# Kernel tuning notes

Measured on AMD Instinct MI355X. Metric: run time of the kernel, lower is better.

## Reference

```python
import jax, jax.numpy as jnp
import numpy as np

T = 2048
D_MODEL = 4096
N_HEADS = 32
N_GROUPS = 8
HEAD_DIM = 128


def _rope_tables(tokens, head_dim, base=10000.0):
    inv_freq = 1.0 / (base ** (np.arange(0, head_dim, 2, dtype=np.float32) / head_dim))
    pos = np.arange(tokens, dtype=np.float32)
    freqs = np.einsum('t,d->td', pos, inv_freq)          # [T, D/2]
    emb = np.concatenate([freqs, freqs], axis=-1)         # [T, D]
    return jnp.asarray(np.cos(emb)), jnp.asarray(np.sin(emb))


def setup_inputs() -> dict:
    key = jax.random.key(0)
    k1, k2, k3 = jax.random.split(key, 3)
    x = jax.random.normal(k1, (T, D_MODEL), dtype=jnp.float32)
    w_qkv = jax.random.normal(k2, (D_MODEL, (N_HEADS + 2 * N_GROUPS) * HEAD_DIM), dtype=jnp.float32) * 0.02
    w_out = jax.random.normal(k3, (N_HEADS * HEAD_DIM, D_MODEL), dtype=jnp.float32) * 0.02
    cos, sin = _rope_tables(T, HEAD_DIM)
    mask = jnp.tril(jnp.ones((T, T), dtype=bool))  # causal: [suffix_tokens, total_tokens]
    return {"x": x, "w_qkv": w_qkv, "w_out": w_out, "cos": cos, "sin": sin, "mask": mask}


def _rotate_half(u):
    u1, u2 = jnp.split(u, 2, axis=-1)
    return jnp.concatenate([-u2, u1], axis=-1)


def _apply_rope(u, cos, sin):
    # u: [tokens, heads, head_dim]; cos/sin: [tokens, head_dim]
    c = cos[:, None, :]
    s = sin[:, None, :]
    return u * c + _rotate_half(u) * s


def reference(x, w_qkv, w_out, cos, sin, mask):
    group_dim = N_HEADS // N_GROUPS
    qkv = x @ w_qkv                                        # [T, (H+2G)*D]
    q, k, v = jnp.split(qkv, [N_HEADS * HEAD_DIM, (N_HEADS + N_GROUPS) * HEAD_DIM], axis=-1)
    q = q.reshape(T, N_HEADS, HEAD_DIM)
    k = k.reshape(T, N_GROUPS, HEAD_DIM)
    v = v.reshape(T, N_GROUPS, HEAD_DIM)
    q = _apply_rope(q, cos, sin)
    k = _apply_rope(k, cos, sin)
    # GQA: group queries -> [T, G, group_dim, D]
    qg = q.reshape(T, N_GROUPS, group_dim, HEAD_DIM)
    scale = 1.0 / jnp.sqrt(jnp.asarray(HEAD_DIM, dtype=q.dtype))
    scores = jnp.einsum('tghd,sgd->ghts', qg, k) * scale   # [G, gd, T, S]
    neg = jnp.asarray(jnp.finfo(scores.dtype).min, scores.dtype)
    scores = jnp.where(mask[None, None, :, :], scores, neg)
    probs = jax.nn.softmax(scores, axis=-1)
    out = jnp.einsum('ghts,sgd->tghd', probs, v)           # [T, G, gd, D]
    out = out.reshape(T, N_HEADS * HEAD_DIM)
    return out @ w_out                                     # [T, model_dim]
```

## Files before the change

kernel.cpp:

```cpp
#include <hip/hip_runtime.h>
#include <cstdint>
#include <cstddef>

#define TT   2048
#define DM   4096
#define NH   32
#define NG   8
#define HD   128
#define QKVN 6144
#define KOFF 4096
#define VOFF 5120

typedef __attribute__((ext_vector_type(8))) short bf16x8;
typedef __attribute__((ext_vector_type(4))) float f32x4;
typedef unsigned short u16;

__device__ __forceinline__ u16 f2b(float f) {
  unsigned u = __builtin_bit_cast(unsigned, f);
  u += 0x7fffu + ((u >> 16) & 1u);
  return (u16)(u >> 16);
}
__device__ __forceinline__ float b2f(u16 s) {
  unsigned u = ((unsigned)s) << 16;
  return __builtin_bit_cast(float, u);
}

__device__ __forceinline__ void gload_lds16(const void* g, void* l) {
  __builtin_amdgcn_global_load_lds(
      (const __attribute__((address_space(1))) unsigned int*)g,
      (__attribute__((address_space(3))) unsigned int*)l,
      16, 0, 0);
}

__global__ __launch_bounds__(256) void cvt_f32_bf16(
    const float* __restrict__ src, u16* __restrict__ dst, int n) {
  for (int i = (blockIdx.x * 256 + threadIdx.x) * 4; i < n; i += gridDim.x * 256 * 4) {
    float4 v = *(const float4*)(src + i);
    ushort4 o;
    o.x = f2b(v.x); o.y = f2b(v.y); o.z = f2b(v.z); o.w = f2b(v.w);
    *(ushort4*)(dst + i) = o;
  }
}

__global__ __launch_bounds__(256) void transpose_cvt(
    const float* __restrict__ src, u16* __restrict__ dst, int R, int C) {
  __shared__ __align__(16) u16 tile[64 * 68];
  const int rb = blockIdx.y * 64, cb = blockIdx.x * 64;
  const int tid = threadIdx.x;
#pragma unroll
  for (int it = 0; it < 4; ++it) {
    const int idx = it * 256 + tid;
    const int r = idx >> 4, c4 = (idx & 15) * 4;
    const float4 v = *(const float4*)(src + (size_t)(rb + r) * C + cb + c4);
    tile[(c4 + 0) * 68 + r] = f2b(v.x);
    tile[(c4 + 1) * 68 + r] = f2b(v.y);
    tile[(c4 + 2) * 68 + r] = f2b(v.z);
    tile[(c4 + 3) * 68 + r] = f2b(v.w);
  }
  __syncthreads();
#pragma unroll
  for (int it = 0; it < 4; ++it) {
    const int idx = it * 256 + tid;
    const int c = idx >> 4, r4 = (idx & 15) * 4;
    const ushort4 o = *(const ushort4*)&tile[c * 68 + r4];
    *(ushort4*)(dst + (size_t)(cb + c) * R + rb + r4) = o;
  }
}

template <int WN, bool OUT_BF16>
__global__ __launch_bounds__(512) void gemm8p(
    const u16* __restrict__ A, const u16* __restrict__ Bt, void* __restrict__ Cout,
    int M, int N, int K) {
  __shared__ __align__(16) u16 sA[2][128 * 64];
  __shared__ __align__(16) u16 sB[2][WN * 64 * 64];
  const int tid = threadIdx.x;
  const int wid = tid >> 6, lane = tid & 63;
  const int lane15 = lane & 15, laneh = lane >> 4;
  const int wm = wid >> 2, wn = wid & 3;
  const int bid = blockIdx.x;
  const int xcd = bid & 7, j = bid >> 3;
  const int m0 = ((xcd >> 1) * 4 + (j >> 3)) * 128;
  const int n0 = ((xcd & 1) * 8 + (j & 7)) * (WN * 64);
  const int xorL = (lane15 & 7) << 3;

  f32x4 acc[4][WN];
#pragma unroll
  for (int m = 0; m < 4; ++m)
#pragma unroll
    for (int n = 0; n < WN; ++n)
#pragma unroll
      for (int r = 0; r < 4; ++r) acc[m][n][r] = 0.f;

  auto stageA = [&](int buf, int t) {
    const int k0 = t << 6;
#pragma unroll
    for (int i = 0; i < 2; ++i) {
      const int ebase = (wid * 2 + i) * 512;
      const int e = ebase + lane * 8;
      const int row = e >> 6;
      const int col = (e & 63) ^ ((row & 7) << 3);
      gload_lds16(A + (size_t)(m0 + row) * K + k0 + col, &sA[buf][ebase]);
    }
  };
  auto stageB = [&](int buf, int t) {
    const int k0 = t << 6;
#pragma unroll
    for (int i = 0; i < WN; ++i) {
      const int ebase = (wid * WN + i) * 512;
      const int e = ebase + lane * 8;
      const int row = e >> 6;
      const int col = (e & 63) ^ ((row & 7) << 3);
      gload_lds16(Bt + (size_t)(n0 + row) * K + k0 + col, &sB[buf][ebase]);
    }
  };

  const int NT = K >> 6;
  stageA(0, 0);
  stageB(0, 0);
  stageA(1, 1);
  asm volatile("s_waitcnt vmcnt(2)");
  __builtin_amdgcn_s_barrier();

  for (int u = 0; u < NT; ++u) {
    const int cur = u & 1;
    bf16x8 af[4][2], bfr[WN][2];
#pragma unroll
    for (int m = 0; m < 4; ++m)
#pragma unroll
      for (int ks = 0; ks < 2; ++ks)
        af[m][ks] = *(const bf16x8*)&sA[cur][(wm * 64 + m * 16 + lane15) * 64 +
                                            ((ks * 32 + laneh * 8) ^ xorL)];
#pragma unroll
    for (int n = 0; n < WN / 2; ++n)
#pragma unroll
      for (int ks = 0; ks < 2; ++ks)
        bfr[n][ks] = *(const bf16x8*)&sB[cur][(wn * (WN * 16) + n * 16 + lane15) * 64 +
                                             ((ks * 32 + laneh * 8) ^ xorL)];
    if (u + 1 < NT) stageB(cur ^ 1, u + 1);
    __builtin_amdgcn_sched_barrier(0);
    __builtin_amdgcn_s_setprio(1);
#pragma unroll
    for (int ks = 0; ks < 2; ++ks)
#pragma unroll
      for (int m = 0; m < 4; ++m)
#pragma unroll
        for (int n = 0; n < WN / 2; ++n)
          acc[m][n] = __builtin_amdgcn_mfma_f32_16x16x32_bf16(af[m][ks], bfr[n][ks], acc[m][n], 0, 0, 0);
    __builtin_amdgcn_s_setprio(0);
    __builtin_amdgcn_s_barrier();
#pragma unroll
    for (int n = WN / 2; n < WN; ++n)
#pragma unroll
      for (int ks = 0; ks < 2; ++ks)
        bfr[n][ks] = *(const bf16x8*)&sB[cur][(wn * (WN * 16) + n * 16 + lane15) * 64 +
                                             ((ks * 32 + laneh * 8) ^ xorL)];
    if (u + 2 < NT) stageA(cur, u + 2);
    __builtin_amdgcn_sched_barrier(0);
    __builtin_amdgcn_s_setprio(1);
#pragma unroll
    for (int ks = 0; ks < 2; ++ks)
#pragma unroll
      for (int m = 0; m < 4; ++m)
#pragma unroll
        for (int n = WN / 2; n < WN; ++n)
          acc[m][n] = __builtin_amdgcn_mfma_f32_16x16x32_bf16(af[m][ks], bfr[n][ks], acc[m][n], 0, 0, 0);
    __builtin_amdgcn_s_setprio(0);
    if (u + 2 < NT) asm volatile("s_waitcnt vmcnt(2)");
    else            asm volatile("s_waitcnt vmcnt(0)");
    __builtin_amdgcn_s_barrier();
  }
#pragma unroll
  for (int m = 0; m < 4; ++m)
#pragma unroll
    for (int n = 0; n < WN; ++n)
#pragma unroll
      for (int r = 0; r < 4; ++r) {
        const int row = m0 + wm * 64 + m * 16 + laneh * 4 + r;
        const int col = n0 + wn * (WN * 16) + n * 16 + lane15;
        const float v = acc[m][n][r];
        if (OUT_BF16) ((u16*)Cout)[(size_t)row * N + col] = f2b(v);
        else          ((float*)Cout)[(size_t)row * N + col] = v;
      }
}

__global__ __launch_bounds__(256) void rope_rearrange(
    const u16* __restrict__ qkv, const float* __restrict__ cosT,
    const float* __restrict__ sinT, u16* __restrict__ Qr, u16* __restrict__ Kr) {
  const int u = blockIdx.x * 4 + (threadIdx.x >> 6);
  const int lane = threadIdx.x & 63;
  const int t = u & (TT - 1);
  const int e = u >> 11;
  const u16* in;
  u16* outp;
  if (e < NH) {
    in = qkv + (size_t)t * QKVN + e * HD;
    outp = Qr + ((size_t)e * TT + t) * HD;
  } else {
    const int g = e - NH;
    in = qkv + (size_t)t * QKVN + KOFF + g * HD;
    outp = Kr + ((size_t)g * TT + t) * HD;
  }
  const float u1 = b2f(in[lane]), u2 = b2f(in[lane + 64]);
  const float c1 = cosT[t * HD + lane], s1 = sinT[t * HD + lane];
  const float c2 = cosT[t * HD + lane + 64], s2 = sinT[t * HD + lane + 64];
  outp[lane]      = f2b(u1 * c1 - u2 * s1);
  outp[lane + 64] = f2b(u2 * c2 + u1 * s2);
}

__global__ __launch_bounds__(256) void vtrans(
    const u16* __restrict__ qkv, u16* __restrict__ VT) {
  __shared__ u16 tile[64][66];
  const int g = blockIdx.z;
  const int t0 = blockIdx.x * 64, d0 = blockIdx.y * 64;
  const int tid = threadIdx.x;
#pragma unroll
  for (int it = 0; it < 16; ++it) {
    int idx = it * 256 + tid;
    int i = idx >> 6, j = idx & 63;
    tile[i][j] = qkv[(size_t)(t0 + i) * QKVN + VOFF + g * HD + d0 + j];
  }
  __syncthreads();
#pragma unroll
  for (int it = 0; it < 16; ++it) {
    int idx = it * 256 + tid;
    int j = idx >> 6, i = idx & 63;
    VT[((size_t)g * HD + d0 + j) * TT + t0 + i] = tile[i][j];
  }
}

__global__ __launch_bounds__(512)
__attribute__((amdgpu_waves_per_eu(1, 2)))
void attn(
    const u16* __restrict__ Qr, const u16* __restrict__ Kr,
    const u16* __restrict__ VT, u16* __restrict__ AO) {
  __shared__ __align__(16) u16 sK[2][128 * 128];
  __shared__ __align__(16) u16 sV[2][128 * 128];
  __shared__ __align__(16) u16 sP[8][32 * 64];
  const int bid = blockIdx.x;
  const int swz = (bid & 7) * 32 + (bid >> 3);
  const int h = swz >> 3, p = swz & 7;
  const int g = h >> 2;
  const int tid = threadIdx.x, wid = tid >> 6, lane = tid & 63;
  const int lane15 = lane & 15, laneh = lane >> 4;
  const int qw = wid >> 1, sw = wid & 1;
  const int xorL = (lane15 & 7) << 3;
  const u16* Qh = Qr + (size_t)h * TT * HD;
  const u16* Kg = Kr + (size_t)g * TT * HD;
  const u16* Vg = VT + (size_t)g * HD * TT;
  const float scale = 0.08838834764831845f;
  float* mlbuf = (float*)&sP[0][0];
  float* obuf  = (float*)&sK[0][0];

  auto stageKV = [&](int buf, int kv) {
#pragma unroll
    for (int i = 0; i < 4; ++i) {
      const int ebase = (wid * 4 + i) * 512;
      const int e = ebase + lane * 8;
      const int row = e >> 7;
      const int col = (e & 127) ^ ((row & 7) << 3);
      gload_lds16(Kg + (size_t)(kv * 128 + row) * HD + col, &sK[buf][ebase]);
      gload_lds16(Vg + (size_t)row * TT + kv * 128 + col, &sV[buf][ebase]);
    }
  };

  for (int pass = 0; pass < 2; ++pass) {
    const int qt = pass ? (15 - p) : p;
    bf16x8 qf[2][4];
    const int qrow0 = qt * 128 + qw * 32;
#pragma unroll
    for (int m = 0; m < 2; ++m)
#pragma unroll
      for (int ks = 0; ks < 4; ++ks)
        qf[m][ks] = *(const bf16x8*)(Qh + (size_t)(qrow0 + m * 16 + lane15) * HD + ks * 32 + laneh * 8);

    f32x4 acc[2][8];
    float mrow[2][4], lrow[2][4];
#pragma unroll
    for (int m = 0; m < 2; ++m) {
#pragma unroll
      for (int n = 0; n < 8; ++n)
#pragma unroll
        for (int r = 0; r < 4; ++r) acc[m][n][r] = 0.f;
#pragma unroll
      for (int r = 0; r < 4; ++r) { mrow[m][r] = -1e30f; lrow[m][r] = 0.f; }
    }

    stageKV(0, 0);
    for (int kv = 0; kv <= qt; ++kv) {
      const int cur = kv & 1;
      if (kv < qt) stageKV(cur ^ 1, kv + 1);
      __builtin_amdgcn_sched_barrier(0);
      if (kv < qt) asm volatile("s_waitcnt vmcnt(8)");
      else         asm volatile("s_waitcnt vmcnt(0)");
      __builtin_amdgcn_s_barrier();

      f32x4 s[2][4];
#pragma unroll
      for (int m = 0; m < 2; ++m)
#pragma unroll
        for (int n = 0; n < 4; ++n)
#pragma unroll
          for (int r = 0; r < 4; ++r) s[m][n][r] = 0.f;
      __builtin_amdgcn_s_setprio(1);
#pragma unroll
      for (int ks = 0; ks < 4; ++ks) {
        bf16x8 kf[4];
#pragma unroll
        for (int n = 0; n < 4; ++n)
          kf[n] = *(const bf16x8*)&sK[cur][(sw * 64 + n * 16 + lane15) * 128 +
                                          ((ks * 32 + laneh * 8) ^ xorL)];
#pragma unroll
        for (int m = 0; m < 2; ++m)
#pragma unroll
          for (int n = 0; n < 4; ++n)
            s[m][n] = __builtin_amdgcn_mfma_f32_16x16x32_bf16(qf[m][ks], kf[n], s[m][n], 0, 0, 0);
      }
      __builtin_amdgcn_s_setprio(0);

      if (kv == qt) {
#pragma unroll
        for (int m = 0; m < 2; ++m)
#pragma unroll
          for (int n = 0; n < 4; ++n)
#pragma unroll
            for (int r = 0; r < 4; ++r) {
              const int ql = qw * 32 + m * 16 + laneh * 4 + r;
              const int sl = sw * 64 + n * 16 + lane15;
              s[m][n][r] = (sl > ql) ? -1e30f : s[m][n][r] * scale;
            }
      } else {
#pragma unroll
        for (int m = 0; m < 2; ++m)
#pragma unroll
          for (int n = 0; n < 4; ++n)
#pragma unroll
            for (int r = 0; r < 4; ++r) s[m][n][r] *= scale;
      }
#pragma unroll
      for (int m = 0; m < 2; ++m)
#pragma unroll
        for (int r = 0; r < 4; ++r) {
          float pm = s[m][0][r];
#pragma unroll
          for (int n = 1; n < 4; ++n) pm = fmaxf(pm, s[m][n][r]);
          pm = fmaxf(pm, __shfl_xor(pm, 1));
          pm = fmaxf(pm, __shfl_xor(pm, 2));
          pm = fmaxf(pm, __shfl_xor(pm, 4));
          pm = fmaxf(pm, __shfl_xor(pm, 8));
          const float mnew = fmaxf(mrow[m][r], pm);
          const float corr = __expf(mrow[m][r] - mnew);
          mrow[m][r] = mnew;
          float ps = 0.f;
#pragma unroll
          for (int n = 0; n < 4; ++n) {
            const float pr = __expf(s[m][n][r] - mnew);
            s[m][n][r] = pr;
            ps += pr;
          }
          ps += __shfl_xor(ps, 1); ps += __shfl_xor(ps, 2);
          ps += __shfl_xor(ps, 4); ps += __shfl_xor(ps, 8);
          lrow[m][r] = lrow[m][r] * corr + ps;
#pragma unroll
          for (int n = 0; n < 8; ++n) acc[m][n][r] *= corr;
        }
#pragma unroll
      for (int m = 0; m < 2; ++m)
#pragma unroll
        for (int n = 0; n < 4; ++n)
#pragma unroll
          for (int r = 0; r < 4; ++r) {
            const int prow = m * 16 + laneh * 4 + r;
            const int pcol = (n * 16 + lane15) ^ ((prow & 7) << 3);
            sP[wid][prow * 64 + pcol] = f2b(s[m][n][r]);
          }
      __builtin_amdgcn_s_setprio(1);
#pragma unroll
      for (int ks = 0; ks < 2; ++ks) {
        bf16x8 pf[2];
#pragma unroll
        for (int m = 0; m < 2; ++m)
          pf[m] = *(const bf16x8*)&sP[wid][(m * 16 + lane15) * 64 + ((ks * 32 + laneh * 8) ^ xorL)];
#pragma unroll
        for (int nh = 0; nh < 2; ++nh) {
          bf16x8 vf[4];
#pragma unroll
          for (int n = 0; n < 4; ++n)
            vf[n] = *(const bf16x8*)&sV[cur][((nh * 4 + n) * 16 + lane15) * 128 +
                                            ((sw * 64 + ks * 32 + laneh * 8) ^ xorL)];
#pragma unroll
          for (int m = 0; m < 2; ++m)
#pragma unroll
            for (int n = 0; n < 4; ++n)
              acc[m][nh * 4 + n] =
                  __builtin_amdgcn_mfma_f32_16x16x32_bf16(pf[m], vf[n], acc[m][nh * 4 + n], 0, 0, 0);
        }
      }
      __builtin_amdgcn_s_setprio(0);
      __builtin_amdgcn_s_barrier();
    }

    if (lane15 == 0) {
#pragma unroll
      for (int m = 0; m < 2; ++m)
#pragma unroll
        for (int r = 0; r < 4; ++r) {
          const int row = m * 16 + laneh * 4 + r;
          mlbuf[(qw * 2 + sw) * 32 + row] = mrow[m][r];
          mlbuf[256 + (qw * 2 + sw) * 32 + row] = lrow[m][r];
        }
    }
    __builtin_amdgcn_s_barrier();
    float sc[2][4], Lr[2][4];
#pragma unroll
    for (int m = 0; m < 2; ++m)
#pragma unroll
      for (int r = 0; r < 4; ++r) {
        const int row = m * 16 + laneh * 4 + r;
        const float mp = mlbuf[(qw * 2 + (sw ^ 1)) * 32 + row];
        const float lp = mlbuf[256 + (qw * 2 + (sw ^ 1)) * 32 + row];
        const float M = fmaxf(mrow[m][r], mp);
        sc[m][r] = __expf(mrow[m][r] - M);
        Lr[m][r] = lrow[m][r] * sc[m][r] + lp * __expf(mp - M);
      }
    if (sw == 0) {
#pragma unroll
      for (int m = 0; m < 2; ++m)
#pragma unroll
        for (int n = 0; n < 8; ++n)
#pragma unroll
          for (int r = 0; r < 4; ++r) {
            const int row = m * 16 + laneh * 4 + r;
            const int col = (n * 16 + lane15) ^ ((row & 7) << 3);
            obuf[qw * 4096 + row * 128 + col] = acc[m][n][r] * sc[m][r];
          }
    }
    __builtin_amdgcn_s_barrier();
    if (sw == 1) {
#pragma unroll
      for (int m = 0; m < 2; ++m)
#pragma unroll
        for (int n = 0; n < 8; ++n)
#pragma unroll
          for (int r = 0; r < 4; ++r) {
            const int row = m * 16 + laneh * 4 + r;
            const int col = (n * 16 + lane15) ^ ((row & 7) << 3);
            const float o = obuf[qw * 4096 + row * 128 + col] + acc[m][n][r] * sc[m][r];
            const int trow = qt * 128 + qw * 32 + row;
            AO[(size_t)trow * DM + h * HD + n * 16 + lane15] = f2b(o / Lr[m][r]);
          }
    }
    __builtin_amdgcn_s_barrier();
  }
}

extern "C" void kernel_launch(void* const* d_in, const int* in_sizes, int n_in,
                              void* d_out, int out_size, void* d_ws, size_t ws_size,
                              hipStream_t stream) {
  const float* x     = (const float*)d_in[0];
  const float* w_qkv = (const float*)d_in[1];
  const float* w_out = (const float*)d_in[2];
  const float* cosT  = (const float*)d_in[3];
  const float* sinT  = (const float*)d_in[4];
  float* out = (float*)d_out;

  char* ws = (char*)d_ws;
  u16* wT  = (u16*)(ws);
  u16* xb  = (u16*)(ws + 50331648);
  u16* qkv = (u16*)(ws + 50331648 + 16777216);
  u16* Qr  = (u16*)(ws + 50331648 + 16777216 + 25165824);
  u16* Kr  = Qr + (size_t)NH * TT * HD;
  u16* VT  = Kr + (size_t)NG * TT * HD;
  u16* AO  = xb;

  cvt_f32_bf16<<<2048, 256, 0, stream>>>(x, xb, TT * DM);
  transpose_cvt<<<dim3(QKVN / 64, DM / 64), 256, 0, stream>>>(w_qkv, wT, DM, QKVN);
  gemm8p<6, true><<<dim3((TT / 128) * (QKVN / 384)), 512, 0, stream>>>(
      xb, wT, qkv, TT, QKVN, DM);
  rope_rearrange<<<(TT * (NH + NG)) / 4, 256, 0, stream>>>(qkv, cosT, sinT, Qr, Kr);
  vtrans<<<dim3(TT / 64, HD / 64, NG), 256, 0, stream>>>(qkv, VT);
  transpose_cvt<<<dim3(DM / 64, DM / 64), 256, 0, stream>>>(w_out, wT, DM, DM);
  attn<<<NH * 8, 512, 0, stream>>>(Qr, Kr, VT, AO);
  gemm8p<4, false><<<dim3((TT / 128) * (DM / 256)), 512, 0, stream>>>(
      AO, wT, out, TT, DM, DM);
}
```

Before: 390.7 us.

## Restructure attention into 512 single-tile blocks with 64-wide KV steps, no cross-wave merge

The attention kernel now launches one 256-thread block per (head, query tile), 512 blocks in total. Before, 256 blocks of 512 threads each handled two query tiles and split every KV tile between two wave halves. KV tiles shrink to 64 keys, so each wave covers the whole KV slice, and the LDS-based merge of partial softmax states and outputs goes away. This removes the cross-wave reduction and its barriers, and the smaller LDS footprint should let more blocks run per CU. In exchange the kernel runs twice as many KV iterations, each with its own barrier, and causal load balance now depends on block scheduling rather than the paired tiles inside one block.

```diff
diff --git a/kernel.cpp b/kernel.cpp
--- a/kernel.cpp
+++ b/kernel.cpp
@@ -10,6 +10,7 @@
 #define QKVN 6144
 #define KOFF 4096
 #define VOFF 5120
+#define KVB  64
 
 typedef __attribute__((ext_vector_type(8))) short bf16x8;
 typedef __attribute__((ext_vector_type(4))) float f32x4;
@@ -228,228 +229,188 @@
   }
 }
 
-__global__ __launch_bounds__(512)
-__attribute__((amdgpu_waves_per_eu(1, 2)))
-void attn(
+__global__ __launch_bounds__(256) void attn(
     const u16* __restrict__ Qr, const u16* __restrict__ Kr,
     const u16* __restrict__ VT, u16* __restrict__ AO) {
-  __shared__ __align__(16) u16 sK[2][128 * 128];
-  __shared__ __align__(16) u16 sV[2][128 * 128];
-  __shared__ __align__(16) u16 sP[8][32 * 64];
+  __shared__ __align__(16) u16 sK[2][KVB * 128];
+  __shared__ __align__(16) u16 sV[2][128 * KVB];
+  __shared__ __align__(16) u16 sP[4][32 * KVB];
   const int bid = blockIdx.x;
-  const int swz = (bid & 7) * 32 + (bid >> 3);
+  const int half = bid >> 8, rem = bid & 255;
+  const int swz = (rem & 7) * 32 + (rem >> 3);
   const int h = swz >> 3, p = swz & 7;
+  const int qt = half ? (15 - p) : p;
   const int g = h >> 2;
   const int tid = threadIdx.x, wid = tid >> 6, lane = tid & 63;
   const int lane15 = lane & 15, laneh = lane >> 4;
-  const int qw = wid >> 1, sw = wid & 1;
   const int xorL = (lane15 & 7) << 3;
   const u16* Qh = Qr + (size_t)h * TT * HD;
   const u16* Kg = Kr + (size_t)g * TT * HD;
   const u16* Vg = VT + (size_t)g * HD * TT;
   const float scale = 0.08838834764831845f;
-  float* mlbuf = (float*)&sP[0][0];
-  float* obuf  = (float*)&sK[0][0];
 
   auto stageKV = [&](int buf, int kv) {
 #pragma unroll
     for (int i = 0; i < 4; ++i) {
       const int ebase = (wid * 4 + i) * 512;
       const int e = ebase + lane * 8;
-      const int row = e >> 7;
-      const int col = (e & 127) ^ ((row & 7) << 3);
-      gload_lds16(Kg + (size_t)(kv * 128 + row) * HD + col, &sK[buf][ebase]);
-      gload_lds16(Vg + (size_t)row * TT + kv * 128 + col, &sV[buf][ebase]);
+      {
+        const int row = e >> 7, col = (e & 127) ^ ((row & 7) << 3);
+        gload_lds16(Kg + (size_t)(kv * KVB + row) * HD + col, &sK[buf][ebase]);
+      }
+      {
+        const int row = e >> 6, col = (e & 63) ^ ((row & 7) << 3);
+        gload_lds16(Vg + (size_t)row * TT + kv * KVB + col, &sV[buf][ebase]);
+      }
     }
   };
 
-  for (int pass = 0; pass < 2; ++pass) {
-    const int qt = pass ? (15 - p) : p;
-    bf16x8 qf[2][4];
-    const int qrow0 = qt * 128 + qw * 32;
+  bf16x8 qf[2][4];
+  const int qrow0 = qt * 128 + wid * 32;
+#pragma unroll
+  for (int m = 0; m < 2; ++m)
+#pragma unroll
+    for (int ks = 0; ks < 4; ++ks)
+      qf[m][ks] = *(const bf16x8*)(Qh + (size_t)(qrow0 + m * 16 + lane15) * HD + ks * 32 + laneh * 8);
+
+  f32x4 acc[2][8];
+  float mrow[2][4], lrow[2][4];
+#pragma unroll
+  for (int m = 0; m < 2; ++m) {
+#pragma unroll
+    for (int n = 0; n < 8; ++n)
+#pragma unroll
+      for (int r = 0; r < 4; ++r) acc[m][n][r] = 0.f;
+#pragma unroll
+    for (int r = 0; r < 4; ++r) { mrow[m][r] = -1e30f; lrow[m][r] = 0.f; }
+  }
+
+  const int NKV = 2 * qt + 2;
+  stageKV(0, 0);
+  for (int kv = 0; kv < NKV; ++kv) {
+    const int cur = kv & 1;
+    if (kv + 1 < NKV) stageKV(cur ^ 1, kv + 1);
+    __builtin_amdgcn_sched_barrier(0);
+    if (kv + 1 < NKV) asm volatile("s_waitcnt vmcnt(8)");
+    else              asm volatile("s_waitcnt vmcnt(0)");
+    __builtin_amdgcn_s_barrier();
+
+    f32x4 s[2][4];
 #pragma unroll
     for (int m = 0; m < 2; ++m)
 #pragma unroll
-      for (int ks = 0; ks < 4; ++ks)
-        qf[m][ks] = *(const bf16x8*)(Qh + (size_t)(qrow0 + m * 16 + lane15) * HD + ks * 32 + laneh * 8);
-
-    f32x4 acc[2][8];
-    float mrow[2][4], lrow[2][4];
-#pragma unroll
-    for (int m = 0; m < 2; ++m) {
-#pragma unroll
-      for (int n = 0; n < 8; ++n)
-#pragma unroll
-        for (int r = 0; r < 4; ++r) acc[m][n][r] = 0.f;
-#pragma unroll
-      for (int r = 0; r < 4; ++r) { mrow[m][r] = -1e30f; lrow[m][r] = 0.f; }
-    }
-
-    stageKV(0, 0);
-    for (int kv = 0; kv <= qt; ++kv) {
-      const int cur = kv & 1;
-      if (kv < qt) stageKV(cur ^ 1, kv + 1);
-      __builtin_amdgcn_sched_barrier(0);
-      if (kv < qt) asm volatile("s_waitcnt vmcnt(8)");
-      else         asm volatile("s_waitcnt vmcnt(0)");
-      __builtin_amdgcn_s_barrier();
-
-      f32x4 s[2][4];
+      for (int n = 0; n < 4; ++n)
+#pragma unroll
+        for (int r = 0; r < 4; ++r) s[m][n][r] = 0.f;
+    __builtin_amdgcn_s_setprio(1);
+#pragma unroll
+    for (int ks = 0; ks < 4; ++ks) {
+      bf16x8 kf[4];
+#pragma unroll
+      for (int n = 0; n < 4; ++n)
+        kf[n] = *(const bf16x8*)&sK[cur][(n * 16 + lane15) * 128 + ((ks * 32 + laneh * 8) ^ xorL)];
 #pragma unroll
       for (int m = 0; m < 2; ++m)
 #pragma unroll
         for (int n = 0; n < 4; ++n)
-#pragma unroll
-          for (int r = 0; r < 4; ++r) s[m][n][r] = 0.f;
-      __builtin_amdgcn_s_setprio(1);
-#pragma unroll
-      for (int ks = 0; ks < 4; ++ks) {
-        bf16x8 kf[4];
+          s[m][n] = __builtin_amdgcn_mfma_f32_16x16x32_bf16(qf[m][ks], kf[n], s[m][n], 0, 0, 0);
+    }
+    __builtin_amdgcn_s_setprio(0);
+
+    const int c = kv - 2 * qt;
+    if (c >= 0) {
+#pragma unroll
+      for (int m = 0; m < 2; ++m)
 #pragma unroll
         for (int n = 0; n < 4; ++n)
-          kf[n] = *(const bf16x8*)&sK[cur][(sw * 64 + n * 16 + lane15) * 128 +
+#pragma unroll
+          for (int r = 0; r < 4; ++r) {
+            const int ql = wid * 32 + m * 16 + laneh * 4 + r;
+            const int sl = c * 64 + n * 16 + lane15;
+            s[m][n][r] = (sl > ql) ? -1e30f : s[m][n][r] * scale;
+          }
+    } else {
+#pragma unroll
+      for (int m = 0; m < 2; ++m)
+#pragma unroll
+        for (int n = 0; n < 4; ++n)
+#pragma unroll
+          for (int r = 0; r < 4; ++r) s[m][n][r] *= scale;
+    }
+#pragma unroll
+    for (int m = 0; m < 2; ++m)
+#pragma unroll
+      for (int r = 0; r < 4; ++r) {
+        float pm = s[m][0][r];
+#pragma unroll
+        for (int n = 1; n < 4; ++n) pm = fmaxf(pm, s[m][n][r]);
+        pm = fmaxf(pm, __shfl_xor(pm, 1));
+        pm = fmaxf(pm, __shfl_xor(pm, 2));
+        pm = fmaxf(pm, __shfl_xor(pm, 4));
+        pm = fmaxf(pm, __shfl_xor(pm, 8));
+        const float mnew = fmaxf(mrow[m][r], pm);
+        const float corr = __expf(mrow[m][r] - mnew);
+        mrow[m][r] = mnew;
+        float ps = 0.f;
+#pragma unroll
+        for (int n = 0; n < 4; ++n) {
+          const float pr = __expf(s[m][n][r] - mnew);
+          s[m][n][r] = pr;
+          ps += pr;
+        }
+        ps += __shfl_xor(ps, 1); ps += __shfl_xor(ps, 2);
+        ps += __shfl_xor(ps, 4); ps += __shfl_xor(ps, 8);
+        lrow[m][r] = lrow[m][r] * corr + ps;
+#pragma unroll
+        for (int n = 0; n < 8; ++n) acc[m][n][r] *= corr;
+      }
+#pragma unroll
+    for (int m = 0; m < 2; ++m)
+#pragma unroll
+      for (int n = 0; n < 4; ++n)
+#pragma unroll
+        for (int r = 0; r < 4; ++r) {
+          const int prow = m * 16 + laneh * 4 + r;
+          const int pcol = (n * 16 + lane15) ^ ((prow & 7) << 3);
+          sP[wid][prow * KVB + pcol] = f2b(s[m][n][r]);
+        }
+    __builtin_amdgcn_s_setprio(1);
+#pragma unroll
+    for (int ks = 0; ks < 2; ++ks) {
+      bf16x8 pf[2];
+#pragma unroll
+      for (int m = 0; m < 2; ++m)
+        pf[m] = *(const bf16x8*)&sP[wid][(m * 16 + lane15) * KVB + ((ks * 32 + laneh * 8) ^ xorL)];
+#pragma unroll
+      for (int nh = 0; nh < 2; ++nh) {
+        bf16x8 vf[4];
+#pragma unroll
+        for (int n = 0; n < 4; ++n)
+          vf[n] = *(const bf16x8*)&sV[cur][((nh * 4 + n) * 16 + lane15) * KVB +
                                           ((ks * 32 + laneh * 8) ^ xorL)];
 #pragma unroll
         for (int m = 0; m < 2; ++m)
 #pragma unroll
           for (int n = 0; n < 4; ++n)
-            s[m][n] = __builtin_amdgcn_mfma_f32_16x16x32_bf16(qf[m][ks], kf[n], s[m][n], 0, 0, 0);
-      }
-      __builtin_amdgcn_s_setprio(0);
-
-      if (kv == qt) {
-#pragma unroll
-        for (int m = 0; m < 2; ++m)
-#pragma unroll
-          for (int n = 0; n < 4; ++n)
-#pragma unroll
-            for (int r = 0; r < 4; ++r) {
-              const int ql = qw * 32 + m * 16 + laneh * 4 + r;
-              const int sl = sw * 64 + n * 16 + lane15;
-              s[m][n][r] = (sl > ql) ? -1e30f : s[m][n][r] * scale;
-            }
-      } else {
-#pragma unroll
-        for (int m = 0; m < 2; ++m)
-#pragma unroll
-          for (int n = 0; n < 4; ++n)
-#pragma unroll
-            for (int r = 0; r < 4; ++r) s[m][n][r] *= scale;
-      }
-#pragma unroll
-      for (int m = 0; m < 2; ++m)
-#pragma unroll
-        for (int r = 0; r < 4; ++r) {
-          float pm = s[m][0][r];
-#pragma unroll
-          for (int n = 1; n < 4; ++n) pm = fmaxf(pm, s[m][n][r]);
-          pm = fmaxf(pm, __shfl_xor(pm, 1));
-          pm = fmaxf(pm, __shfl_xor(pm, 2));
-          pm = fmaxf(pm, __shfl_xor(pm, 4));
-          pm = fmaxf(pm, __shfl_xor(pm, 8));
-          const float mnew = fmaxf(mrow[m][r], pm);
-          const float corr = __expf(mrow[m][r] - mnew);
-          mrow[m][r] = mnew;
-          float ps = 0.f;
-#pragma unroll
-          for (int n = 0; n < 4; ++n) {
-            const float pr = __expf(s[m][n][r] - mnew);
-            s[m][n][r] = pr;
-            ps += pr;
-          }
-          ps += __shfl_xor(ps, 1); ps += __shfl_xor(ps, 2);
-          ps += __shfl_xor(ps, 4); ps += __shfl_xor(ps, 8);
-          lrow[m][r] = lrow[m][r] * corr + ps;
-#pragma unroll
-          for (int n = 0; n < 8; ++n) acc[m][n][r] *= corr;
-        }
-#pragma unroll
-      for (int m = 0; m < 2; ++m)
-#pragma unroll
-        for (int n = 0; n < 4; ++n)
-#pragma unroll
-          for (int r = 0; r < 4; ++r) {
-            const int prow = m * 16 + laneh * 4 + r;
-            const int pcol = (n * 16 + lane15) ^ ((prow & 7) << 3);
-            sP[wid][prow * 64 + pcol] = f2b(s[m][n][r]);
-          }
-      __builtin_amdgcn_s_setprio(1);
-#pragma unroll
-      for (int ks = 0; ks < 2; ++ks) {
-        bf16x8 pf[2];
-#pragma unroll
-        for (int m = 0; m < 2; ++m)
-          pf[m] = *(const bf16x8*)&sP[wid][(m * 16 + lane15) * 64 + ((ks * 32 + laneh * 8) ^ xorL)];
-#pragma unroll
-        for (int nh = 0; nh < 2; ++nh) {
-          bf16x8 vf[4];
-#pragma unroll
-          for (int n = 0; n < 4; ++n)
-            vf[n] = *(const bf16x8*)&sV[cur][((nh * 4 + n) * 16 + lane15) * 128 +
-                                            ((sw * 64 + ks * 32 + laneh * 8) ^ xorL)];
-#pragma unroll
-          for (int m = 0; m < 2; ++m)
-#pragma unroll
-            for (int n = 0; n < 4; ++n)
-              acc[m][nh * 4 + n] =
-                  __builtin_amdgcn_mfma_f32_16x16x32_bf16(pf[m], vf[n], acc[m][nh * 4 + n], 0, 0, 0);
-        }
-      }
-      __builtin_amdgcn_s_setprio(0);
-      __builtin_amdgcn_s_barrier();
-    }
-
-    if (lane15 == 0) {
-#pragma unroll
-      for (int m = 0; m < 2; ++m)
-#pragma unroll
-        for (int r = 0; r < 4; ++r) {
-          const int row = m * 16 + laneh * 4 + r;
-          mlbuf[(qw * 2 + sw) * 32 + row] = mrow[m][r];
-          mlbuf[256 + (qw * 2 + sw) * 32 + row] = lrow[m][r];
-        }
-    }
+            acc[m][nh * 4 + n] =
+                __builtin_amdgcn_mfma_f32_16x16x32_bf16(pf[m], vf[n], acc[m][nh * 4 + n], 0, 0, 0);
+      }
+    }
+    __builtin_amdgcn_s_setprio(0);
     __builtin_amdgcn_s_barrier();
-    float sc[2][4], Lr[2][4];
-#pragma unroll
-    for (int m = 0; m < 2; ++m)
+  }
+#pragma unroll
+  for (int m = 0; m < 2; ++m) {
+    float inv[4];
+#pragma unroll
+    for (int r = 0; r < 4; ++r) inv[r] = 1.f / lrow[m][r];
+#pragma unroll
+    for (int n = 0; n < 8; ++n)
 #pragma unroll
       for (int r = 0; r < 4; ++r) {
-        const int row = m * 16 + laneh * 4 + r;
-        const float mp = mlbuf[(qw * 2 + (sw ^ 1)) * 32 + row];
-        const float lp = mlbuf[256 + (qw * 2 + (sw ^ 1)) * 32 + row];
-        const float M = fmaxf(mrow[m][r], mp);
-        sc[m][r] = __expf(mrow[m][r] - M);
-        Lr[m][r] = lrow[m][r] * sc[m][r] + lp * __expf(mp - M);
-      }
-    if (sw == 0) {
-#pragma unroll
-      for (int m = 0; m < 2; ++m)
-#pragma unroll
-        for (int n = 0; n < 8; ++n)
-#pragma unroll
-          for (int r = 0; r < 4; ++r) {
-            const int row = m * 16 + laneh * 4 + r;
-            const int col = (n * 16 + lane15) ^ ((row & 7) << 3);
-            obuf[qw * 4096 + row * 128 + col] = acc[m][n][r] * sc[m][r];
-          }
-    }
-    __builtin_amdgcn_s_barrier();
-    if (sw == 1) {
-#pragma unroll
-      for (int m = 0; m < 2; ++m)
-#pragma unroll
-        for (int n = 0; n < 8; ++n)
-#pragma unroll
-          for (int r = 0; r < 4; ++r) {
-            const int row = m * 16 + laneh * 4 + r;
-            const int col = (n * 16 + lane15) ^ ((row & 7) << 3);
-            const float o = obuf[qw * 4096 + row * 128 + col] + acc[m][n][r] * sc[m][r];
-            const int trow = qt * 128 + qw * 32 + row;
-            AO[(size_t)trow * DM + h * HD + n * 16 + lane15] = f2b(o / Lr[m][r]);
-          }
-    }
-    __builtin_amdgcn_s_barrier();
+        const int trow = qt * 128 + wid * 32 + m * 16 + laneh * 4 + r;
+        AO[(size_t)trow * DM + h * HD + n * 16 + lane15] = f2b(acc[m][n][r] * inv[r]);
+      }
   }
 }
 
@@ -479,7 +440,7 @@
   rope_rearrange<<<(TT * (NH + NG)) / 4, 256, 0, stream>>>(qkv, cosT, sinT, Qr, Kr);
   vtrans<<<dim3(TT / 64, HD / 64, NG), 256, 0, stream>>>(qkv, VT);
   transpose_cvt<<<dim3(DM / 64, DM / 64), 256, 0, stream>>>(w_out, wT, DM, DM);
-  attn<<<NH * 8, 512, 0, stream>>>(Qr, Kr, VT, AO);
+  attn<<<NH * 16, 256, 0, stream>>>(Qr, Kr, VT, AO);
   gemm8p<4, false><<<dim3((TT / 128) * (DM / 256)), 512, 0, stream>>>(
       AO, wT, out, TT, DM, DM);
 }
```

Result: slower. 405.1 us (+3.7%).
